# Performance work log

Measured on AMD Instinct MI355X. Metric: run time of the kernel, lower is better.

## Reference

```python
import jax, jax.numpy as jnp
from jax import lax
import numpy as np

T, B, X, Y = 24, 16, 32, 32
FS, FM, FC = 64, 16, 16
I = FS + FM + FC  # GRU input size = 96
H = 32            # hidden_size


def setup_inputs() -> dict:
    key = jax.random.key(0)
    ks = jax.random.split(key, 8)
    s = 1.0 / np.sqrt(H)  # pytorch GRU init scale
    return {
        "spatial": jax.random.normal(ks[0], (B, X, Y, FS), jnp.float32),
        "meteorology": jax.random.normal(ks[1], (T, B, X, Y, FM), jnp.float32),
        "context": jax.random.normal(ks[2], (T, B, X, Y, FC), jnp.float32),
        "W_ih": jax.random.uniform(ks[3], (3 * H, I), jnp.float32, -s, s),
        "W_hh": jax.random.uniform(ks[4], (3 * H, H), jnp.float32, -s, s),
        "b_ih": jax.random.uniform(ks[5], (3 * H,), jnp.float32, -s, s),
        "b_hh": jax.random.uniform(ks[6], (3 * H,), jnp.float32, -s, s),
        "W": jax.random.normal(ks[7], (H, FS), jnp.float32),
    }


def _gru_final_state(x, W_ih, W_hh, b_ih, b_hh):
    # x: (T, N, I); returns final hidden state (N, H). PyTorch GRU cell math.
    n_batch = x.shape[1]
    h0 = jnp.zeros((n_batch, H), x.dtype)

    def step(h, xt):
        gi = xt @ W_ih.T + b_ih          # (N, 3H)
        gh = h @ W_hh.T + b_hh           # (N, 3H)
        i_r, i_z, i_n = jnp.split(gi, 3, axis=-1)
        h_r, h_z, h_n = jnp.split(gh, 3, axis=-1)
        r = jax.nn.sigmoid(i_r + h_r)
        z = jax.nn.sigmoid(i_z + h_z)
        n = jnp.tanh(i_n + r * h_n)
        h_new = (1.0 - z) * n + z * h
        return h_new, None

    hT, _ = lax.scan(step, h0, x)
    return hT


def reference(spatial, meteorology, context, W_ih, W_hh, b_ih, b_hh, W):
    # Broadcast static spatial features over time and concat along feature dim.
    t = meteorology.shape[0]
    sp = jnp.broadcast_to(spatial[None], (t,) + spatial.shape)
    x = jnp.concatenate([sp, meteorology, context], axis=-1)  # (T,B,X,Y,I)
    # Batch all spatial positions into one recurrence: (T, B*X*Y, I)
    x = x.reshape(t, B * X * Y, I)
    hT = _gru_final_state(x, W_ih, W_hh, b_ih, b_hh)          # (B*X*Y, H)
    out = hT @ W                                              # (B*X*Y, FS)
    return out.reshape(B, X, Y, FS)
```

## Files before the change

### kernel.cpp

```cpp
#include <hip/hip_runtime.h>
#include <hip/hip_fp16.h>
#include <math.h>


typedef __attribute__((ext_vector_type(8))) _Float16 half8;
typedef __attribute__((ext_vector_type(4))) float f32x4;
typedef __attribute__((ext_vector_type(4))) unsigned int uix4;

#define NSEQ 16384
#define TSTEPS 24
#define NINT 12
#define LOG2E 1.44269504088896340736f

__device__ __forceinline__ float exp2_fast(float x) {
#if __has_builtin(__builtin_amdgcn_exp2f)
  return __builtin_amdgcn_exp2f(x);
#else
  return __expf(x * 0.6931471805599453f);
#endif
}

__device__ __forceinline__ unsigned int pk_f16(float a, float b) {
#if __has_builtin(__builtin_amdgcn_cvt_pkrtz)
  auto r = __builtin_amdgcn_cvt_pkrtz(a, b);
  return __builtin_bit_cast(unsigned int, r);
#else
  return (unsigned)__half_as_ushort(__float2half(a)) |
         ((unsigned)__half_as_ushort(__float2half(b)) << 16);
#endif
}
__device__ __forceinline__ unsigned int pk_f16_rn(float a, float b) {
  return (unsigned)__half_as_ushort(__float2half(a)) |
         ((unsigned)__half_as_ushort(__float2half(b)) << 16);
}
__device__ __forceinline__ half8 mk_h8(unsigned int a, unsigned int b,
                                       unsigned int c, unsigned int d) {
  uix4 v = {a, b, c, d};
  return __builtin_bit_cast(half8, v);
}
__device__ __forceinline__ f32x4 mfma_h(half8 a, half8 b, f32x4 c) {
  return __builtin_amdgcn_mfma_f32_16x16x32_f16(a, b, c, 0, 0, 0);
}

__device__ __forceinline__ void barrier_lds() {
  asm volatile("s_waitcnt lgkmcnt(0)" ::: "memory");
  __builtin_amdgcn_s_barrier();
}

__global__ __launch_bounds__(128, 4)
void gru11(const float* __restrict__ spatial,
           const float* __restrict__ met,
           const float* __restrict__ ctx,
           const float* __restrict__ W_ih,
           const float* __restrict__ W_hh,
           const float* __restrict__ b_ih,
           const float* __restrict__ b_hh,
           const float* __restrict__ Wp,
           float* __restrict__ out) {
  __shared__ float xls[2][2][6][16][20];

  const int tid = threadIdx.x;
  const int lane = tid & 63;
  const int wv = tid >> 6;
  const int l15 = lane & 15;
  const int c = lane >> 4;
  const int seq = blockIdx.x * 16 + l15;
  const f32x4 zero4 = {0.f, 0.f, 0.f, 0.f};

  if (wv == 1) {
    half8 wmc[6];
    f32x4 acc_i[6];
#pragma unroll
    for (int j = 0; j < 6; ++j) {
      const float sc = (j < 4) ? LOG2E : (2.0f * LOG2E);
      const float* mr = W_ih + (size_t)(j * 16 + l15) * 96 + 64 + c * 8;
      float4 wa = *(const float4*)mr;
      float4 wb = *(const float4*)(mr + 4);
      wmc[j] = mk_h8(pk_f16_rn(wa.x * sc, wa.y * sc),
                     pk_f16_rn(wa.z * sc, wa.w * sc),
                     pk_f16_rn(wb.x * sc, wb.y * sc),
                     pk_f16_rn(wb.z * sc, wb.w * sc));
      const int rowb = j * 16 + 4 * c;
      float4 vih = *(const float4*)(b_ih + rowb);
      if (j < 4) {
        float4 vhh = *(const float4*)(b_hh + rowb);
        acc_i[j][0] = (vih.x + vhh.x) * sc; acc_i[j][1] = (vih.y + vhh.y) * sc;
        acc_i[j][2] = (vih.z + vhh.z) * sc; acc_i[j][3] = (vih.w + vhh.w) * sc;
      } else {
        acc_i[j][0] = vih.x * sc; acc_i[j][1] = vih.y * sc;
        acc_i[j][2] = vih.z * sc; acc_i[j][3] = vih.w * sc;
      }
    }
#pragma unroll
    for (int kt = 0; kt < 2; ++kt) {
      const float* sp = spatial + (size_t)seq * 64 + kt * 32 + c * 8;
      float4 a0 = *(const float4*)sp;
      float4 a1 = *(const float4*)(sp + 4);
      half8 sf = mk_h8(pk_f16(a0.x, a0.y), pk_f16(a0.z, a0.w),
                       pk_f16(a1.x, a1.y), pk_f16(a1.z, a1.w));
#pragma unroll
      for (int j = 0; j < 6; ++j) {
        const float sc = (j < 4) ? LOG2E : (2.0f * LOG2E);
        const float* wr = W_ih + (size_t)(j * 16 + l15) * 96 + kt * 32 + c * 8;
        float4 wa = *(const float4*)wr;
        float4 wb = *(const float4*)(wr + 4);
        half8 wsp = mk_h8(pk_f16_rn(wa.x * sc, wa.y * sc),
                          pk_f16_rn(wa.z * sc, wa.w * sc),
                          pk_f16_rn(wb.x * sc, wb.y * sc),
                          pk_f16_rn(wb.z * sc, wb.w * sc));
        acc_i[j] = mfma_h(wsp, sf, acc_i[j]);
      }
    }
    const float* lptr = ((c < 2) ? met : ctx) + (size_t)seq * 16 + (c & 1) * 8;

    auto fill = [&](int buf, int s, float4 xa, float4 xb) {
      half8 xf = mk_h8(pk_f16(xa.x, xa.y), pk_f16(xa.z, xa.w),
                       pk_f16(xb.x, xb.y), pk_f16(xb.z, xb.w));
#pragma unroll
      for (int j = 0; j < 6; ++j) {
        f32x4 D = mfma_h(wmc[j], xf, acc_i[j]);
        *(f32x4*)&xls[buf][s][j][l15][c * 4] = D;
      }
    };
    auto ldx = [&](int t, float4& a, float4& b) {
      const float* p = lptr + (size_t)t * NSEQ * 16;
      a = *(const float4*)p; b = *(const float4*)(p + 4);
    };

    {
      float4 a0, b0, a1, b1;
      ldx(0, a0, b0); ldx(1, a1, b1);
      fill(0, 0, a0, b0); fill(0, 1, a1, b1);
    }
    float4 c0a, c0b, c1a, c1b, n0a, n0b, n1a, n1b;
    ldx(2, c0a, c0b); ldx(3, c1a, c1b);
    ldx(4, n0a, n0b); ldx(5, n1a, n1b);

#pragma unroll 2
    for (int k = 0; k < NINT; ++k) {
      barrier_lds();
      if (k < NINT - 1) {
        fill((k + 1) & 1, 0, c0a, c0b);
        fill((k + 1) & 1, 1, c1a, c1b);
        c0a = n0a; c0b = n0b; c1a = n1a; c1b = n1b;
        int t0 = (2 * k + 6 < TSTEPS) ? (2 * k + 6) : (TSTEPS - 1);
        int t1 = (2 * k + 7 < TSTEPS) ? (2 * k + 7) : (TSTEPS - 1);
        ldx(t0, n0a, n0b); ldx(t1, n1a, n1b);
      }
    }
  } else {
    __builtin_amdgcn_s_setprio(1);
    half8 whh[6];
#pragma unroll
    for (int j = 0; j < 6; ++j) {
      const float sc = (j < 4) ? LOG2E : (2.0f * LOG2E);
      const float* wr = W_hh + (size_t)(j * 16 + l15) * 32;
      float4 a = *(const float4*)(wr + 4 * c);
      float4 b = *(const float4*)(wr + 16 + 4 * c);
      whh[j] = mk_h8(pk_f16_rn(a.x * sc, a.y * sc),
                     pk_f16_rn(a.z * sc, a.w * sc),
                     pk_f16_rn(b.x * sc, b.y * sc),
                     pk_f16_rn(b.z * sc, b.w * sc));
    }
    f32x4 bhnA, bhnB;
    {
      float4 va = *(const float4*)(b_hh + 64 + 4 * c);
      float4 vb = *(const float4*)(b_hh + 64 + 16 + 4 * c);
      bhnA[0] = 2.0f * LOG2E * va.x; bhnA[1] = 2.0f * LOG2E * va.y;
      bhnA[2] = 2.0f * LOG2E * va.z; bhnA[3] = 2.0f * LOG2E * va.w;
      bhnB[0] = 2.0f * LOG2E * vb.x; bhnB[1] = 2.0f * LOG2E * vb.y;
      bhnB[2] = 2.0f * LOG2E * vb.z; bhnB[3] = 2.0f * LOG2E * vb.w;
    }
    float hst[8];
#pragma unroll
    for (int i = 0; i < 8; ++i) hst[i] = 0.0f;
    half8 fh = mk_h8(0u, 0u, 0u, 0u);

    auto do_step = [&](f32x4 xr0, f32x4 xr1, f32x4 xz0, f32x4 xz1,
                       f32x4 ti0, f32x4 ti1) {
      f32x4 dr0 = mfma_h(whh[0], fh, xr0);
      f32x4 dr1 = mfma_h(whh[1], fh, xr1);
      f32x4 dz0 = mfma_h(whh[2], fh, xz0);
      f32x4 dz1 = mfma_h(whh[3], fh, xz1);
      f32x4 th0 = mfma_h(whh[4], fh, bhnA);
      f32x4 th1 = mfma_h(whh[5], fh, bhnB);
      float hv_[8];
#pragma unroll
      for (int jj = 0; jj < 2; ++jj) {
        f32x4 ddr = jj ? dr1 : dr0;
        f32x4 ddz = jj ? dz1 : dz0;
        f32x4 tth = jj ? th1 : th0;
        f32x4 tti = jj ? ti1 : ti0;
#pragma unroll
        for (int q = 0; q < 4; ++q) {
          const int i = jj * 4 + q;
          float R = exp2_fast(-ddr[q]);
          float r = __builtin_amdgcn_rcpf(1.0f + R);
          float E = fminf(exp2_fast(-ddz[q]), 1e30f);
          float Y = fmaf(r, tth[q], tti[q]);
          float e = fminf(exp2_fast(-Y), 1e30f);
          float oe = 1.0f + e, oE = 1.0f + E;
          float inv = __builtin_amdgcn_rcpf(oE * oe);
          float num = fmaf(hst[i], oe, fmaf(-E, e, E));
          float hv = num * inv;
          hst[i] = hv;
          hv_[i] = hv;
        }
      }
      fh = mk_h8(pk_f16(hv_[0], hv_[1]), pk_f16(hv_[2], hv_[3]),
                 pk_f16(hv_[4], hv_[5]), pk_f16(hv_[6], hv_[7]));
    };

#pragma unroll 2
    for (int k = 0; k < NINT; ++k) {
      const int buf = k & 1;
      barrier_lds();
      f32x4 A0 = *(const f32x4*)&xls[buf][0][0][l15][c * 4];
      f32x4 A1 = *(const f32x4*)&xls[buf][0][1][l15][c * 4];
      f32x4 A2 = *(const f32x4*)&xls[buf][0][2][l15][c * 4];
      f32x4 A3 = *(const f32x4*)&xls[buf][0][3][l15][c * 4];
      f32x4 A4 = *(const f32x4*)&xls[buf][0][4][l15][c * 4];
      f32x4 A5 = *(const f32x4*)&xls[buf][0][5][l15][c * 4];
      f32x4 B0 = *(const f32x4*)&xls[buf][1][0][l15][c * 4];
      f32x4 B1 = *(const f32x4*)&xls[buf][1][1][l15][c * 4];
      f32x4 B2 = *(const f32x4*)&xls[buf][1][2][l15][c * 4];
      f32x4 B3 = *(const f32x4*)&xls[buf][1][3][l15][c * 4];
      f32x4 B4 = *(const f32x4*)&xls[buf][1][4][l15][c * 4];
      f32x4 B5 = *(const f32x4*)&xls[buf][1][5][l15][c * 4];
      do_step(A0, A1, A2, A3, A4, A5);
      do_step(B0, B1, B2, B3, B4, B5);
    }

#pragma unroll
    for (int pt = 0; pt < 4; ++pt) {
      const int frow = pt * 16 + l15;
      const float* wpb = Wp + frow;
      float v[8];
#pragma unroll
      for (int e = 0; e < 8; ++e) {
        int col = (e < 4) ? (4 * c + e) : (16 + 4 * c + (e - 4));
        v[e] = wpb[(size_t)col * 64];
      }
      unsigned int uh[4], ul[4];
#pragma unroll
      for (int e2 = 0; e2 < 4; ++e2) {
        float va = v[2 * e2], vb = v[2 * e2 + 1];
        __half ha = __float2half(va), hb = __float2half(vb);
        float la = va - __half2float(ha), lb = vb - __half2float(hb);
        uh[e2] = (unsigned)__half_as_ushort(ha) |
                 ((unsigned)__half_as_ushort(hb) << 16);
        ul[e2] = pk_f16_rn(la, lb);
      }
      half8 wph = mk_h8(uh[0], uh[1], uh[2], uh[3]);
      half8 wpl = mk_h8(ul[0], ul[1], ul[2], ul[3]);
      f32x4 o = mfma_h(wph, fh, zero4);
      o = mfma_h(wpl, fh, o);
      float* op = out + (size_t)seq * 64 + pt * 16 + 4 * c;
      *(float4*)op = make_float4(o[0], o[1], o[2], o[3]);
    }
    __builtin_amdgcn_s_setprio(0);
  }
}

extern "C" void kernel_launch(void* const* d_in, const int* in_sizes, int n_in,
                              void* d_out, int out_size, void* d_ws, size_t ws_size,
                              hipStream_t stream) {
  const float* spatial = (const float*)d_in[0];
  const float* met     = (const float*)d_in[1];
  const float* ctx     = (const float*)d_in[2];
  const float* W_ih    = (const float*)d_in[3];
  const float* W_hh    = (const float*)d_in[4];
  const float* b_ih    = (const float*)d_in[5];
  const float* b_hh    = (const float*)d_in[6];
  const float* Wp      = (const float*)d_in[7];
  float* out = (float*)d_out;

  hipLaunchKernelGGL(gru11, dim3(1024), dim3(128), 0, stream,
                     spatial, met, ctx, W_ih, W_hh, b_ih, b_hh, Wp, out);
}
```

Measured before the change: 25.04 us.

## Use 4-slot LDS ring with per-step barriers and prefetch next step's inputs

Replaces the double-buffered pair-of-steps LDS exchange between the producer wave and the recurrence wave with a 4-slot ring synchronised once per timestep. The recurrence wave now issues the LDS read for the next step before computing the current one, hiding LDS latency behind the gate math. The gate math is also rewritten to use separate reciprocals for z and for the tanh, dropping the clamps and the combined-denominator trick. This doubles the number of barriers per sequence, and the reformulated tanh 2s-1 may lose some precision near zero.

Result: slower. 26.98 us (+7.7%).

```diff
diff --git a/kernel.cpp b/kernel.cpp
--- a/kernel.cpp
+++ b/kernel.cpp
@@ -9,7 +9,6 @@
 
 #define NSEQ 16384
 #define TSTEPS 24
-#define NINT 12
 #define LOG2E 1.44269504088896340736f
 
 __device__ __forceinline__ float exp2_fast(float x) {
@@ -48,7 +47,7 @@
 }
 
 __global__ __launch_bounds__(128, 4)
-void gru11(const float* __restrict__ spatial,
+void gru12(const float* __restrict__ spatial,
            const float* __restrict__ met,
            const float* __restrict__ ctx,
            const float* __restrict__ W_ih,
@@ -57,7 +56,7 @@
            const float* __restrict__ b_hh,
            const float* __restrict__ Wp,
            float* __restrict__ out) {
-  __shared__ float xls[2][2][6][16][20];
+  __shared__ float xls[4][6][16][20];
 
   const int tid = threadIdx.x;
   const int lane = tid & 63;
@@ -113,13 +112,13 @@
     }
     const float* lptr = ((c < 2) ? met : ctx) + (size_t)seq * 16 + (c & 1) * 8;
 
-    auto fill = [&](int buf, int s, float4 xa, float4 xb) {
+    auto fill = [&](int slot, float4 xa, float4 xb) {
       half8 xf = mk_h8(pk_f16(xa.x, xa.y), pk_f16(xa.z, xa.w),
                        pk_f16(xb.x, xb.y), pk_f16(xb.z, xb.w));
 #pragma unroll
       for (int j = 0; j < 6; ++j) {
         f32x4 D = mfma_h(wmc[j], xf, acc_i[j]);
-        *(f32x4*)&xls[buf][s][j][l15][c * 4] = D;
+        *(f32x4*)&xls[slot][j][l15][c * 4] = D;
       }
     };
     auto ldx = [&](int t, float4& a, float4& b) {
@@ -130,22 +129,28 @@
     {
       float4 a0, b0, a1, b1;
       ldx(0, a0, b0); ldx(1, a1, b1);
-      fill(0, 0, a0, b0); fill(0, 1, a1, b1);
-    }
-    float4 c0a, c0b, c1a, c1b, n0a, n0b, n1a, n1b;
-    ldx(2, c0a, c0b); ldx(3, c1a, c1b);
-    ldx(4, n0a, n0b); ldx(5, n1a, n1b);
+      fill(0, a0, b0); fill(1, a1, b1);
+    }
+    float4 pAa, pAb, pBa, pBb;
+    ldx(2, pAa, pAb); ldx(3, pBa, pBb);
+
+    barrier_lds();
 
 #pragma unroll 2
-    for (int k = 0; k < NINT; ++k) {
-      barrier_lds();
-      if (k < NINT - 1) {
-        fill((k + 1) & 1, 0, c0a, c0b);
-        fill((k + 1) & 1, 1, c1a, c1b);
-        c0a = n0a; c0b = n0b; c1a = n1a; c1b = n1b;
-        int t0 = (2 * k + 6 < TSTEPS) ? (2 * k + 6) : (TSTEPS - 1);
-        int t1 = (2 * k + 7 < TSTEPS) ? (2 * k + 7) : (TSTEPS - 1);
-        ldx(t0, n0a, n0b); ldx(t1, n1a, n1b);
+    for (int kk = 0; kk < 12; ++kk) {
+      {
+        const int k = 2 * kk;
+        if (k + 2 < TSTEPS) fill((k + 2) & 3, pAa, pAb);
+        int tf = (k + 4 < TSTEPS) ? (k + 4) : (TSTEPS - 1);
+        ldx(tf, pAa, pAb);
+        barrier_lds();
+      }
+      {
+        const int k = 2 * kk + 1;
+        if (k + 2 < TSTEPS) fill((k + 2) & 3, pBa, pBb);
+        int tf = (k + 4 < TSTEPS) ? (k + 4) : (TSTEPS - 1);
+        ldx(tf, pBa, pBb);
+        barrier_lds();
       }
     }
   } else {
@@ -196,13 +201,13 @@
           const int i = jj * 4 + q;
           float R = exp2_fast(-ddr[q]);
           float r = __builtin_amdgcn_rcpf(1.0f + R);
-          float E = fminf(exp2_fast(-ddz[q]), 1e30f);
+          float E = exp2_fast(-ddz[q]);
+          float z = __builtin_amdgcn_rcpf(1.0f + E);
           float Y = fmaf(r, tth[q], tti[q]);
-          float e = fminf(exp2_fast(-Y), 1e30f);
-          float oe = 1.0f + e, oE = 1.0f + E;
-          float inv = __builtin_amdgcn_rcpf(oE * oe);
-          float num = fmaf(hst[i], oe, fmaf(-E, e, E));
-          float hv = num * inv;
+          float e = exp2_fast(-Y);
+          float s = __builtin_amdgcn_rcpf(1.0f + e);
+          float n = fmaf(2.0f, s, -1.0f);
+          float hv = fmaf(z, hst[i] - n, n);
           hst[i] = hv;
           hv_[i] = hv;
         }
@@ -211,24 +216,44 @@
                  pk_f16(hv_[4], hv_[5]), pk_f16(hv_[6], hv_[7]));
     };
 
+    barrier_lds();
+
+    f32x4 A0, A1, A2, A3, A4, A5, B0, B1, B2, B3, B4, B5;
+    A0 = *(const f32x4*)&xls[0][0][l15][c * 4];
+    A1 = *(const f32x4*)&xls[0][1][l15][c * 4];
+    A2 = *(const f32x4*)&xls[0][2][l15][c * 4];
+    A3 = *(const f32x4*)&xls[0][3][l15][c * 4];
+    A4 = *(const f32x4*)&xls[0][4][l15][c * 4];
+    A5 = *(const f32x4*)&xls[0][5][l15][c * 4];
+
 #pragma unroll 2
-    for (int k = 0; k < NINT; ++k) {
-      const int buf = k & 1;
-      barrier_lds();
-      f32x4 A0 = *(const f32x4*)&xls[buf][0][0][l15][c * 4];
-      f32x4 A1 = *(const f32x4*)&xls[buf][0][1][l15][c * 4];
-      f32x4 A2 = *(const f32x4*)&xls[buf][0][2][l15][c * 4];
-      f32x4 A3 = *(const f32x4*)&xls[buf][0][3][l15][c * 4];
-      f32x4 A4 = *(const f32x4*)&xls[buf][0][4][l15][c * 4];
-      f32x4 A5 = *(const f32x4*)&xls[buf][0][5][l15][c * 4];
-      f32x4 B0 = *(const f32x4*)&xls[buf][1][0][l15][c * 4];
-      f32x4 B1 = *(const f32x4*)&xls[buf][1][1][l15][c * 4];
-      f32x4 B2 = *(const f32x4*)&xls[buf][1][2][l15][c * 4];
-      f32x4 B3 = *(const f32x4*)&xls[buf][1][3][l15][c * 4];
-      f32x4 B4 = *(const f32x4*)&xls[buf][1][4][l15][c * 4];
-      f32x4 B5 = *(const f32x4*)&xls[buf][1][5][l15][c * 4];
-      do_step(A0, A1, A2, A3, A4, A5);
-      do_step(B0, B1, B2, B3, B4, B5);
+    for (int kk = 0; kk < 12; ++kk) {
+      {
+        const int k = 2 * kk;
+        const int sl = (k + 1) & 3;
+        B0 = *(const f32x4*)&xls[sl][0][l15][c * 4];
+        B1 = *(const f32x4*)&xls[sl][1][l15][c * 4];
+        B2 = *(const f32x4*)&xls[sl][2][l15][c * 4];
+        B3 = *(const f32x4*)&xls[sl][3][l15][c * 4];
+        B4 = *(const f32x4*)&xls[sl][4][l15][c * 4];
+        B5 = *(const f32x4*)&xls[sl][5][l15][c * 4];
+        do_step(A0, A1, A2, A3, A4, A5);
+        barrier_lds();
+      }
+      {
+        const int k = 2 * kk + 1;
+        if (k + 1 < TSTEPS) {
+          const int sl = (k + 1) & 3;
+          A0 = *(const f32x4*)&xls[sl][0][l15][c * 4];
+          A1 = *(const f32x4*)&xls[sl][1][l15][c * 4];
+          A2 = *(const f32x4*)&xls[sl][2][l15][c * 4];
+          A3 = *(const f32x4*)&xls[sl][3][l15][c * 4];
+          A4 = *(const f32x4*)&xls[sl][4][l15][c * 4];
+          A5 = *(const f32x4*)&xls[sl][5][l15][c * 4];
+        }
+        do_step(B0, B1, B2, B3, B4, B5);
+        barrier_lds();
+      }
     }
 
 #pragma unroll
@@ -275,6 +300,6 @@
   const float* Wp      = (const float*)d_in[7];
   float* out = (float*)d_out;
 
-  hipLaunchKernelGGL(gru11, dim3(1024), dim3(128), 0, stream,
+  hipLaunchKernelGGL(gru12, dim3(1024), dim3(128), 0, stream,
                      spatial, met, ctx, W_ih, W_hh, b_ih, b_hh, Wp, out);
 }
```
